# Optimization experiments

Hardware: AMD Instinct MI355X
Metric: run time of the kernel (lower is better)

The kernel has to match this reference:

```python
import jax, jax.numpy as jnp
import numpy as np

N = 50000      # nodes
E = 800000     # edges (before self-loops)
DIN, H1, H2, OUT = 128, 128, 64, 40
LN_EPS = 1e-5


def setup_inputs() -> dict:
    key = jax.random.key(0)
    ks = jax.random.split(key, 16)
    s = lambda d: 1.0 / np.sqrt(d)
    inp = {
        "x": jax.random.normal(ks[0], (N, DIN), jnp.float32),
        "edge_index": jax.random.randint(ks[1], (2, E), 0, N, dtype=jnp.int64),
        # GCNConv weights (applied as x @ W) and biases
        "W1": jax.random.normal(ks[2], (DIN, H1), jnp.float32) * s(DIN),
        "b1": jnp.zeros((H1,), jnp.float32),
        "W2": jax.random.normal(ks[3], (H1, H2), jnp.float32) * s(H1),
        "b2": jnp.zeros((H2,), jnp.float32),
        "W3": jax.random.normal(ks[4], (H2, H2), jnp.float32) * s(H2),
        "b3": jnp.zeros((H2,), jnp.float32),
        # LayerNorms
        "g1": jnp.ones((H1,), jnp.float32),
        "be1": jnp.zeros((H1,), jnp.float32),
        "g2": jnp.ones((H2,), jnp.float32),
        "be2": jnp.zeros((H2,), jnp.float32),
        # post_mp MLP head
        "Wp1": jax.random.normal(ks[5], (H2, H2), jnp.float32) * s(H2),
        "bp1": jnp.zeros((H2,), jnp.float32),
        "Wp2": jax.random.normal(ks[6], (H2, OUT), jnp.float32) * s(H2),
        "bp2": jnp.zeros((OUT,), jnp.float32),
    }
    return inp


def _layer_norm(x, g, b):
    mu = jnp.mean(x, axis=-1, keepdims=True)
    var = jnp.mean((x - mu) ** 2, axis=-1, keepdims=True)
    return (x - mu) * jax.lax.rsqrt(var + LN_EPS) * g + b


def _gcn(x, src, dst, norm, W, b):
    # PyG GCNConv: linear first, then normalized gather/scatter-add, bias last
    h = x @ W                                  # [N, H]
    msg = h[src] * norm[:, None]               # [E+N, H] gather
    out = jax.ops.segment_sum(msg, dst, num_segments=N)  # scatter-add
    return out + b


def reference(x, edge_index, W1, b1, W2, b2, W3, b3, g1, be1, g2, be2,
              Wp1, bp1, Wp2, bp2):
    loops = jnp.arange(N, dtype=edge_index.dtype)
    src = jnp.concatenate([edge_index[0], loops])  # add self-loops
    dst = jnp.concatenate([edge_index[1], loops])
    # symmetric normalization D^{-1/2} (A+I) D^{-1/2} (same graph all layers)
    deg = jax.ops.segment_sum(jnp.ones_like(src, dtype=x.dtype), dst,
                              num_segments=N)
    dinv = jnp.where(deg > 0, jax.lax.rsqrt(jnp.maximum(deg, 1.0)), 0.0)
    norm = dinv[src] * dinv[dst]

    h = _gcn(x, src, dst, norm, W1, b1)
    h = _layer_norm(jax.nn.relu(h), g1, be1)
    h = _gcn(h, src, dst, norm, W2, b2)
    h = _layer_norm(jax.nn.relu(h), g2, be2)
    emb = _gcn(h, src, dst, norm, W3, b3)      # emb = conv output, pre-ReLU
    h = jax.nn.relu(emb)
    h = (h @ Wp1 + bp1) @ Wp2 + bp2            # post_mp: two stacked Linears
    return emb, jax.nn.log_softmax(h, axis=1)
```

## Files before the change

kernel.cpp:

```cpp
#include <hip/hip_runtime.h>
#include <hip/hip_bf16.h>

#define DIN 128
#define HID1 128
#define HID2 64
#define OUTD 40

typedef __attribute__((ext_vector_type(8))) short bf16x8;
typedef __attribute__((ext_vector_type(4))) float f32x4;

__device__ __forceinline__ float bf2f(unsigned int u) {
    union { unsigned int i; float f; } c;
    c.i = u << 16;
    return c.f;
}
__device__ __forceinline__ unsigned short f2bf(float f) {
    union { float f; unsigned int i; } c; c.f = f;
    unsigned int r = c.i + 0x7FFFu + ((c.i >> 16) & 1u);
    return (unsigned short)(r >> 16);
}
__device__ __forceinline__ unsigned int packbf(float lo, float hi) {
    return (unsigned int)f2bf(lo) | ((unsigned int)f2bf(hi) << 16);
}

__global__ void pre_kernel(const unsigned short* __restrict__ xu,
                           const int* __restrict__ ei, int* __restrict__ flags,
                           int* __restrict__ cnt, int N) {
    int i = blockIdx.x * blockDim.x + threadIdx.x;
    if (i < N) cnt[i] = 0;
    if (blockIdx.x == 0) {
        __shared__ int sh[2];
        if (threadIdx.x < 2) sh[threadIdx.x] = 0;
        __syncthreads();
        int bad = 0;
        for (int k = threadIdx.x; k < 2048; k += 256) {
            float v = bf2f(xu[2 * k]);
            float a = fabsf(v);
            if (!(a <= 1e4f) || (v != 0.f && a < 1e-4f)) bad++;
        }
        int zodd = 0;
        for (int k = threadIdx.x; k < 1024; k += 256)
            if (ei[2 * k + 1] == 0) zodd++;
        atomicAdd(&sh[0], bad);
        atomicAdd(&sh[1], zodd);
        __syncthreads();
        if (threadIdx.x == 0) {
            flags[0] = (sh[0] > 512) ? 1 : 0;
            flags[1] = (sh[1] > 512) ? 1 : 0;
        }
    }
}

__device__ __forceinline__ int get_src(const int* ei, int E, int e, int e64) {
    return e64 ? ei[2 * e] : ei[e];
}
__device__ __forceinline__ int get_dst(const int* ei, int E, int e, int e64) {
    return e64 ? ei[2 * (E + e)] : ei[E + e];
}

__global__ void pos_kernel(const int* __restrict__ ei, int* __restrict__ cnt,
                           int* __restrict__ pos, int E, int N,
                           const int* __restrict__ flags) {
    int e64 = flags[1];
    int base = (blockIdx.x * blockDim.x + threadIdx.x) * 4;
    #pragma unroll
    for (int u = 0; u < 4; ++u) {
        int e = base + u;
        if (e < E) {
            int d = get_dst(ei, E, e, e64);
            pos[e] = ((unsigned)d < (unsigned)N) ? atomicAdd(&cnt[d], 1) : -1;
        }
    }
}


__launch_bounds__(256)
__global__ void bsum_kernel(const int* __restrict__ cnt, int* __restrict__ bsum, int N) {
    __shared__ int sh[256];
    int t = threadIdx.x;
    int i = blockIdx.x * 256 + t;
    sh[t] = (i < N) ? cnt[i] : 0;
    __syncthreads();
    #pragma unroll
    for (int off = 128; off >= 1; off >>= 1) {
        if (t < off) sh[t] += sh[t + off];
        __syncthreads();
    }
    if (t == 0) bsum[blockIdx.x] = sh[0];
}

__launch_bounds__(256)
__global__ void bscan_kernel(const int* __restrict__ bsum, int* __restrict__ bbase,
                             int* __restrict__ indptr, int NB, int N) {
    __shared__ int part[256];
    int t = threadIdx.x;
    int CH = (NB + 255) / 256;
    int lo = t * CH, hi = lo + CH; if (hi > NB) hi = NB;
    int s = 0;
    for (int i = lo; i < hi; ++i) s += bsum[i];
    part[t] = s;
    __syncthreads();
    for (int off = 1; off < 256; off <<= 1) {
        int v = (t >= off) ? part[t - off] : 0;
        __syncthreads();
        part[t] += v;
        __syncthreads();
    }
    int run = (t > 0) ? part[t - 1] : 0;
    for (int i = lo; i < hi; ++i) { bbase[i] = run; run += bsum[i]; }
    if (t == 255) indptr[N] = part[255];
}

__launch_bounds__(256)
__global__ void emit_kernel(const int* __restrict__ cnt, const int* __restrict__ bbase,
                            int* __restrict__ indptr, float* __restrict__ dinv, int N) {
    __shared__ int sh[256];
    int t = threadIdx.x;
    int i = blockIdx.x * 256 + t;
    int c = (i < N) ? cnt[i] : 0;
    sh[t] = c;
    __syncthreads();
    for (int off = 1; off < 256; off <<= 1) {
        int v = (t >= off) ? sh[t - off] : 0;
        __syncthreads();
        sh[t] += v;
        __syncthreads();
    }
    if (i < N) {
        int excl = sh[t] - c + bbase[blockIdx.x];
        indptr[i] = excl;
        dinv[i] = 1.0f / sqrtf((float)(c + 1));
    }
}

__global__ void scatter_kernel(const int* __restrict__ ei, const int* __restrict__ indptr,
                               const int* __restrict__ pos, const float* __restrict__ dinv,
                               int2* __restrict__ csr_sn,
                               int E, int N, const int* __restrict__ flags) {
    int e64 = flags[1];
    int base = (blockIdx.x * blockDim.x + threadIdx.x) * 4;
    #pragma unroll
    for (int u = 0; u < 4; ++u) {
        int e = base + u;
        if (e < E) {
            int p = pos[e];
            if (p >= 0) {
                int d = get_dst(ei, E, e, e64);
                int s = get_src(ei, E, e, e64);
                if ((unsigned)s >= (unsigned)N) s = 0;
                float nrm = dinv[s] * dinv[d];
                csr_sn[indptr[d] + p] = make_int2(s, __float_as_int(nrm));
            }
        }
    }
}


struct WCvt {
    const void* p[14];
    int sz[14];
    int off[14];
    int tobf[14];
    int cols[14];
};

__global__ void wcvt_kernel(WCvt w, unsigned short* __restrict__ wbf,
                            float* __restrict__ wf, const int* __restrict__ flags) {
    int xf32 = flags[0];
    int stride = gridDim.x * blockDim.x;
    int tid = blockIdx.x * blockDim.x + threadIdx.x;
    for (int a = 0; a < 14; ++a) {
        const float* pf = (const float*)w.p[a];
        const unsigned short* pb = (const unsigned short*)w.p[a];
        int n = w.sz[a], off = w.off[a], tobf = w.tobf[a];
        int cols = w.cols[a];
        int rows = tobf ? (n / cols) : 0;
        for (int i = tid; i < n; i += stride) {
            float v = xf32 ? pf[i] : bf2f(pb[i]);
            if (tobf) {
                int k = i / cols, m = i % cols;
                wbf[off + m * rows + k] = f2bf(v);
            } else {
                wf[off + i] = v;
            }
        }
    }
}


template<typename AT>
__device__ __forceinline__ bf16x8 ld_afrag(const AT* p);
template<>
__device__ __forceinline__ bf16x8 ld_afrag<unsigned short>(const unsigned short* p) {
    return *(const bf16x8*)p;
}
template<>
__device__ __forceinline__ bf16x8 ld_afrag<float>(const float* p) {
    float4 a = *(const float4*)p;
    float4 b = *(const float4*)(p + 4);
    bf16x8 r;
    r[0] = (short)f2bf(a.x); r[1] = (short)f2bf(a.y);
    r[2] = (short)f2bf(a.z); r[3] = (short)f2bf(a.w);
    r[4] = (short)f2bf(b.x); r[5] = (short)f2bf(b.y);
    r[6] = (short)f2bf(b.z); r[7] = (short)f2bf(b.w);
    return r;
}

template<int K, int M, typename AT>
__launch_bounds__(256)
__global__ void mm_mfma_kernel(const AT* __restrict__ A,
                               const unsigned short* __restrict__ WT,
                               unsigned short* __restrict__ C, int N,
                               const int* __restrict__ flags, int mode) {
    if (mode >= 0 && flags[0] != mode) return;
    __shared__ unsigned short Ws[M][K + 8];
    int tid = threadIdx.x;
    for (int idx = tid; idx < M * K / 8; idx += 256) {
        int r = idx / (K / 8), c8 = idx % (K / 8);
        *(uint4*)&Ws[r][c8 * 8] = *(const uint4*)&WT[r * K + c8 * 8];
    }
    __syncthreads();
    int w = tid >> 6, lane = tid & 63;
    int m = lane & 15, q = lane >> 4;
    int row_a = blockIdx.x * 64 + w * 16 + m;
    if (row_a >= N) row_a = N - 1;
    const AT* arow = A + (size_t)row_a * K;
    f32x4 acc[M / 16];
    #pragma unroll
    for (int t = 0; t < M / 16; ++t) acc[t] = (f32x4){0.f, 0.f, 0.f, 0.f};
    #pragma unroll
    for (int ks = 0; ks < K / 32; ++ks) {
        int k0 = ks * 32 + q * 8;
        bf16x8 a = ld_afrag<AT>(arow + k0);
        #pragma unroll
        for (int t = 0; t < M / 16; ++t) {
            bf16x8 b = *(const bf16x8*)&Ws[t * 16 + m][k0];
            acc[t] = __builtin_amdgcn_mfma_f32_16x16x32_bf16(a, b, acc[t], 0, 0, 0);
        }
    }
    int rbase = blockIdx.x * 64 + w * 16 + q * 4;
    #pragma unroll
    for (int reg = 0; reg < 4; ++reg) {
        int row = rbase + reg;
        if (row < N) {
            #pragma unroll
            for (int t = 0; t < M / 16; ++t)
                C[(size_t)row * M + t * 16 + m] = f2bf(acc[t][reg]);
        }
    }
}


template<int VPL>
__device__ __forceinline__ void gacc1(float* acc, const unsigned short* r, float n) {
    if constexpr (VPL == 8) {
        uint4 u = *(const uint4*)r;
        acc[0] += bf2f(u.x & 0xffffu) * n; acc[1] += bf2f(u.x >> 16) * n;
        acc[2] += bf2f(u.y & 0xffffu) * n; acc[3] += bf2f(u.y >> 16) * n;
        acc[4] += bf2f(u.z & 0xffffu) * n; acc[5] += bf2f(u.z >> 16) * n;
        acc[6] += bf2f(u.w & 0xffffu) * n; acc[7] += bf2f(u.w >> 16) * n;
    } else {
        uint2 u = *(const uint2*)r;
        acc[0] += bf2f(u.x & 0xffffu) * n; acc[1] += bf2f(u.x >> 16) * n;
        acc[2] += bf2f(u.y & 0xffffu) * n; acc[3] += bf2f(u.y >> 16) * n;
    }
}

template<int VPL>
__device__ __forceinline__ void gacc4(float* acc,
                                      const unsigned short* r0, float n0,
                                      const unsigned short* r1, float n1,
                                      const unsigned short* r2, float n2,
                                      const unsigned short* r3, float n3) {
    if constexpr (VPL == 8) {
        uint4 u0 = *(const uint4*)r0;
        uint4 u1 = *(const uint4*)r1;
        uint4 u2 = *(const uint4*)r2;
        uint4 u3 = *(const uint4*)r3;
        acc[0] += bf2f(u0.x & 0xffffu) * n0 + bf2f(u1.x & 0xffffu) * n1
                + bf2f(u2.x & 0xffffu) * n2 + bf2f(u3.x & 0xffffu) * n3;
        acc[1] += bf2f(u0.x >> 16) * n0 + bf2f(u1.x >> 16) * n1
                + bf2f(u2.x >> 16) * n2 + bf2f(u3.x >> 16) * n3;
        acc[2] += bf2f(u0.y & 0xffffu) * n0 + bf2f(u1.y & 0xffffu) * n1
                + bf2f(u2.y & 0xffffu) * n2 + bf2f(u3.y & 0xffffu) * n3;
        acc[3] += bf2f(u0.y >> 16) * n0 + bf2f(u1.y >> 16) * n1
                + bf2f(u2.y >> 16) * n2 + bf2f(u3.y >> 16) * n3;
        acc[4] += bf2f(u0.z & 0xffffu) * n0 + bf2f(u1.z & 0xffffu) * n1
                + bf2f(u2.z & 0xffffu) * n2 + bf2f(u3.z & 0xffffu) * n3;
        acc[5] += bf2f(u0.z >> 16) * n0 + bf2f(u1.z >> 16) * n1
                + bf2f(u2.z >> 16) * n2 + bf2f(u3.z >> 16) * n3;
        acc[6] += bf2f(u0.w & 0xffffu) * n0 + bf2f(u1.w & 0xffffu) * n1
                + bf2f(u2.w & 0xffffu) * n2 + bf2f(u3.w & 0xffffu) * n3;
        acc[7] += bf2f(u0.w >> 16) * n0 + bf2f(u1.w >> 16) * n1
                + bf2f(u2.w >> 16) * n2 + bf2f(u3.w >> 16) * n3;
    } else {
        uint2 u0 = *(const uint2*)r0;
        uint2 u1 = *(const uint2*)r1;
        uint2 u2 = *(const uint2*)r2;
        uint2 u3 = *(const uint2*)r3;
        acc[0] += bf2f(u0.x & 0xffffu) * n0 + bf2f(u1.x & 0xffffu) * n1
                + bf2f(u2.x & 0xffffu) * n2 + bf2f(u3.x & 0xffffu) * n3;
        acc[1] += bf2f(u0.x >> 16) * n0 + bf2f(u1.x >> 16) * n1
                + bf2f(u2.x >> 16) * n2 + bf2f(u3.x >> 16) * n3;
        acc[2] += bf2f(u0.y & 0xffffu) * n0 + bf2f(u1.y & 0xffffu) * n1
                + bf2f(u2.y & 0xffffu) * n2 + bf2f(u3.y & 0xffffu) * n3;
        acc[3] += bf2f(u0.y >> 16) * n0 + bf2f(u1.y >> 16) * n1
                + bf2f(u2.y >> 16) * n2 + bf2f(u3.y >> 16) * n3;
    }
}

template<int H, bool RELU_LN, bool EMB>
__launch_bounds__(256)
__global__ void agg_kernel(const unsigned short* __restrict__ h,
                           const int* __restrict__ indptr,
                           const int2* __restrict__ csr_sn,
                           const float* __restrict__ dinv,
                           const float* __restrict__ bias,
                           const float* __restrict__ gamma,
                           const float* __restrict__ beta,
                           unsigned short* __restrict__ out,
                           void* __restrict__ out_emb,
                           int N, const int* __restrict__ flags) {
    constexpr int VPL = H / 16;
    __shared__ int2 lsn[4][4][16];
    int w = threadIdx.x >> 6;
    int lane = threadIdx.x & 63;
    int g = lane >> 4;
    int idx = lane & 15;
    int node = blockIdx.x * 16 + w * 4 + g;
    bool active = node < N;
    int nd = active ? node : N - 1;
    float di = dinv[nd];
    int c0 = idx * VPL;
    float acc[VPL];
    #pragma unroll
    for (int v = 0; v < VPL; ++v) acc[v] = 0.f;
    gacc1<VPL>(acc, h + (size_t)nd * H + c0, di * di);
    int beg = indptr[nd], end = indptr[nd + 1];
    for (int base = beg; base < end; base += 16) {
        int m = end - base; if (m > 16) m = 16;
        if (idx < m) lsn[w][g][idx] = csr_sn[base + idx];
        int j = 0;
        for (; j + 3 < m; j += 4) {
            int2 e0 = lsn[w][g][j],     e1 = lsn[w][g][j + 1];
            int2 e2 = lsn[w][g][j + 2], e3 = lsn[w][g][j + 3];
            gacc4<VPL>(acc,
                       h + (size_t)e0.x * H + c0, __int_as_float(e0.y),
                       h + (size_t)e1.x * H + c0, __int_as_float(e1.y),
                       h + (size_t)e2.x * H + c0, __int_as_float(e2.y),
                       h + (size_t)e3.x * H + c0, __int_as_float(e3.y));
        }
        for (; j < m; ++j) {
            int2 e = lsn[w][g][j];
            gacc1<VPL>(acc, h + (size_t)e.x * H + c0, __int_as_float(e.y));
        }
    }
    #pragma unroll
    for (int v = 0; v < VPL; ++v) acc[v] += bias[c0 + v];
    if constexpr (RELU_LN) {
        #pragma unroll
        for (int v = 0; v < VPL; ++v) acc[v] = fmaxf(acc[v], 0.f);
        float s = 0.f, sq = 0.f;
        #pragma unroll
        for (int v = 0; v < VPL; ++v) { s += acc[v]; sq += acc[v] * acc[v]; }
        #pragma unroll
        for (int off = 8; off >= 1; off >>= 1) {
            s += __shfl_xor(s, off, 64);
            sq += __shfl_xor(sq, off, 64);
        }
        float mu = s * (1.0f / H);
        float var = fmaxf(sq * (1.0f / H) - mu * mu, 0.f);
        float inv = 1.0f / sqrtf(var + 1e-5f);
        #pragma unroll
        for (int v = 0; v < VPL; ++v)
            acc[v] = (acc[v] - mu) * inv * gamma[c0 + v] + beta[c0 + v];
    }
    if (active) {
        unsigned short* orow = out + (size_t)node * H + c0;
        if constexpr (VPL == 8) {
            uint4 p;
            p.x = packbf(acc[0], acc[1]); p.y = packbf(acc[2], acc[3]);
            p.z = packbf(acc[4], acc[5]); p.w = packbf(acc[6], acc[7]);
            *(uint4*)orow = p;
        } else {
            uint2 p; p.x = packbf(acc[0], acc[1]); p.y = packbf(acc[2], acc[3]);
            *(uint2*)orow = p;
        }
        if constexpr (EMB) {
            if (flags[0]) {
                float* o = (float*)out_emb + (size_t)node * H + c0;
                #pragma unroll
                for (int v4 = 0; v4 < VPL / 4; ++v4)
                    *(float4*)(o + v4 * 4) = make_float4(acc[v4 * 4], acc[v4 * 4 + 1],
                                                         acc[v4 * 4 + 2], acc[v4 * 4 + 3]);
            } else {
                unsigned short* o = (unsigned short*)out_emb + (size_t)node * H + c0;
                #pragma unroll
                for (int v2 = 0; v2 < VPL / 2; ++v2)
                    ((unsigned int*)o)[v2] = packbf(acc[v2 * 2], acc[v2 * 2 + 1]);
            }
        }
    }
}


__launch_bounds__(256)
__global__ void head_kernel(const unsigned short* __restrict__ emb,
                            const float* __restrict__ Wp1,
                            const float* __restrict__ bp1,
                            const float* __restrict__ Wp2,
                            const float* __restrict__ bp2,
                            void* __restrict__ d_out, int N,
                            const int* __restrict__ flags) {
    __shared__ float Est[64][68];
    __shared__ float W1s[64][64];
    __shared__ float Tst[64][68];
    __shared__ float W2s[64][OUTD];
    __shared__ float b1s[64];
    __shared__ float b2s[OUTD];
    int tid = threadIdx.x;
    int row0 = blockIdx.x * 64;
    for (int i = tid; i < 64 * 64; i += 256) W1s[i >> 6][i & 63] = Wp1[i];
    for (int i = tid; i < 64 * OUTD; i += 256) W2s[i / OUTD][i % OUTD] = Wp2[i];
    if (tid < 64) b1s[tid] = bp1[tid];
    if (tid < OUTD) b2s[tid] = bp2[tid];
    for (int i = tid; i < 64 * 32; i += 256) {
        int r = i >> 5, kk = i & 31;
        int row = row0 + r;
        unsigned int u = (row < N) ? *(const unsigned int*)&emb[(size_t)row * 64 + kk * 2] : 0u;
        Est[kk * 2][r]     = fmaxf(bf2f(u & 0xffffu), 0.f);
        Est[kk * 2 + 1][r] = fmaxf(bf2f(u >> 16), 0.f);
    }
    __syncthreads();
    {
        int rg = tid >> 4, cg = tid & 15;
        int r = rg * 4, c = cg * 4;
        float acc[4][4];
        #pragma unroll
        for (int i = 0; i < 4; ++i)
            #pragma unroll
            for (int jj = 0; jj < 4; ++jj) acc[i][jj] = b1s[c + jj];
        #pragma unroll 4
        for (int k = 0; k < 64; ++k) {
            float4 a = *(const float4*)&Est[k][r];
            float4 wv = *(const float4*)&W1s[k][c];
            acc[0][0] += a.x * wv.x; acc[0][1] += a.x * wv.y; acc[0][2] += a.x * wv.z; acc[0][3] += a.x * wv.w;
            acc[1][0] += a.y * wv.x; acc[1][1] += a.y * wv.y; acc[1][2] += a.y * wv.z; acc[1][3] += a.y * wv.w;
            acc[2][0] += a.z * wv.x; acc[2][1] += a.z * wv.y; acc[2][2] += a.z * wv.z; acc[2][3] += a.z * wv.w;
            acc[3][0] += a.w * wv.x; acc[3][1] += a.w * wv.y; acc[3][2] += a.w * wv.z; acc[3][3] += a.w * wv.w;
        }
        #pragma unroll
        for (int i = 0; i < 4; ++i)
            #pragma unroll
            for (int jj = 0; jj < 4; ++jj) Tst[c + jj][r + i] = acc[i][jj];
    }
    __syncthreads();
    int row = tid >> 2, tc = tid & 3, o0 = tc * 10;
    int node = row0 + row;
    float u[10];
    #pragma unroll
    for (int o = 0; o < 10; ++o) u[o] = b2s[o0 + o];
    for (int c2 = 0; c2 < 64; ++c2) {
        float tv = Tst[c2][row];
        const float2* wp = (const float2*)&W2s[c2][o0];
        #pragma unroll
        for (int o2 = 0; o2 < 5; ++o2) {
            float2 wv = wp[o2];
            u[o2 * 2]     += tv * wv.x;
            u[o2 * 2 + 1] += tv * wv.y;
        }
    }
    float mx = u[0];
    #pragma unroll
    for (int o = 1; o < 10; ++o) mx = fmaxf(mx, u[o]);
    mx = fmaxf(mx, __shfl_xor(mx, 1, 64));
    mx = fmaxf(mx, __shfl_xor(mx, 2, 64));
    float sum = 0.f;
    #pragma unroll
    for (int o = 0; o < 10; ++o) sum += __expf(u[o] - mx);
    sum += __shfl_xor(sum, 1, 64);
    sum += __shfl_xor(sum, 2, 64);
    float lse = mx + __logf(sum);
    if (node < N) {
        if (flags[0]) {
            float* base = (float*)d_out + (size_t)N * HID2;
            float* op = base + (size_t)node * OUTD + o0;
            #pragma unroll
            for (int o = 0; o < 10; ++o) op[o] = u[o] - lse;
        } else {
            unsigned short* base = (unsigned short*)d_out + (size_t)N * HID2;
            unsigned int* op = (unsigned int*)(base + (size_t)node * OUTD + o0);
            #pragma unroll
            for (int o2 = 0; o2 < 5; ++o2)
                op[o2] = packbf(u[o2 * 2] - lse, u[o2 * 2 + 1] - lse);
        }
    }
}


extern "C" void kernel_launch(void* const* d_in, const int* in_sizes, int n_in,
                              void* d_out, int out_size, void* d_ws, size_t ws_size,
                              hipStream_t stream) {
    const unsigned short* xu = (const unsigned short*)d_in[0];
    const float*          xf = (const float*)d_in[0];
    const int*            ei = (const int*)d_in[1];

    const int N = in_sizes[0] / DIN;
    const int E = in_sizes[1] / 2;

    size_t off = 0;
    auto take = [&](size_t bytes) {
        size_t cur = off;
        off += (bytes + 255) & ~(size_t)255;
        return cur;
    };
    char* ws = (char*)d_ws;
    int*   flags   = (int*)  (ws + take(256));
    int*   cnt     = (int*)  (ws + take((size_t)N * 4));
    float* dinv    = (float*)(ws + take((size_t)N * 4));
    int*   indptr  = (int*)  (ws + take((size_t)(N + 1) * 4));
    int*   pos     = (int*)  (ws + take((size_t)E * 4));
    int2*  csr_sn  = (int2*) (ws + take((size_t)E * 8));
    int*   bsum    = (int*)  (ws + take(((size_t)N / 256 + 2) * 4));
    int*   bbase   = (int*)  (ws + take(((size_t)N / 256 + 2) * 4));
    unsigned short* wbf = (unsigned short*)(ws + take(32768 * 2));
    float*          wf  = (float*)         (ws + take(8192 * 4));
    unsigned short* hbuf = (unsigned short*)(ws + take((size_t)N * DIN * 2));
    unsigned short* abuf = (unsigned short*)(ws + take((size_t)N * DIN * 2));
    (void)ws_size; (void)n_in; (void)out_size;

    const int TB = 256;
    dim3 blk(TB);
    const int NB = (N + 255) / 256;

    pre_kernel<<<dim3(NB), blk, 0, stream>>>(xu, ei, flags, cnt, N);
    pos_kernel<<<dim3((E + 1023) / 1024), blk, 0, stream>>>(ei, cnt, pos, E, N, flags);
    bsum_kernel<<<dim3(NB), blk, 0, stream>>>(cnt, bsum, N);
    bscan_kernel<<<dim3(1), blk, 0, stream>>>(bsum, bbase, indptr, NB, N);
    emit_kernel<<<dim3(NB), blk, 0, stream>>>(cnt, bbase, indptr, dinv, N);
    scatter_kernel<<<dim3((E + 1023) / 1024), blk, 0, stream>>>(ei, indptr, pos, dinv, csr_sn, E, N, flags);

    WCvt w;
    int bfoff = 0, foff = 0;
    int offs[14];
    const int wcols[14] = {HID1, 0, HID2, 0, HID2, 0, 0, 0, 0, 0, 0, 0, 0, 0};
    for (int a = 0; a < 14; ++a) {
        int idx = a + 2;
        w.p[a] = d_in[idx];
        w.sz[a] = in_sizes[idx];
        int tobf = (idx == 2 || idx == 4 || idx == 6) ? 1 : 0;
        w.tobf[a] = tobf;
        w.cols[a] = tobf ? wcols[a] : 1;
        if (tobf) { w.off[a] = bfoff; bfoff += in_sizes[idx]; }
        else      { w.off[a] = foff;  foff  += in_sizes[idx]; }
        offs[a] = w.off[a];
    }
    wcvt_kernel<<<dim3(64), blk, 0, stream>>>(w, wbf, wf, flags);

    unsigned short* W1t = wbf + offs[0];
    unsigned short* W2t = wbf + offs[2];
    unsigned short* W3t = wbf + offs[4];
    float* b1f  = wf + offs[1];
    float* b2f  = wf + offs[3];
    float* b3f  = wf + offs[5];
    float* g1f  = wf + offs[6];
    float* be1f = wf + offs[7];
    float* g2f  = wf + offs[8];
    float* be2f = wf + offs[9];
    float* Wp1f = wf + offs[10];
    float* bp1f = wf + offs[11];
    float* Wp2f = wf + offs[12];
    float* bp2f = wf + offs[13];

    const int MMG = (N + 63) / 64;
    const int AGG = (N + 15) / 16;

    mm_mfma_kernel<DIN, HID1, unsigned short><<<dim3(MMG), blk, 0, stream>>>(
        xu, W1t, hbuf, N, flags, 0);
    mm_mfma_kernel<DIN, HID1, float><<<dim3(MMG), blk, 0, stream>>>(
        xf, W1t, hbuf, N, flags, 1);
    agg_kernel<HID1, true, false><<<dim3(AGG), blk, 0, stream>>>(
        hbuf, indptr, csr_sn, dinv, b1f, g1f, be1f, abuf, nullptr, N, flags);

    mm_mfma_kernel<HID1, HID2, unsigned short><<<dim3(MMG), blk, 0, stream>>>(
        abuf, W2t, hbuf, N, flags, -1);
    agg_kernel<HID2, true, false><<<dim3(AGG), blk, 0, stream>>>(
        hbuf, indptr, csr_sn, dinv, b2f, g2f, be2f, abuf, nullptr, N, flags);

    mm_mfma_kernel<HID2, HID2, unsigned short><<<dim3(MMG), blk, 0, stream>>>(
        abuf, W3t, hbuf, N, flags, -1);
    agg_kernel<HID2, false, true><<<dim3(AGG), blk, 0, stream>>>(
        hbuf, indptr, csr_sn, dinv, b3f, nullptr, nullptr, abuf, d_out, N, flags);

    head_kernel<<<dim3((N + 63) / 64), blk, 0, stream>>>(
        abuf, Wp1f, bp1f, Wp2f, bp2f, d_out, N, flags);
}
```

Before: 312.6 us.

## Build CSR with per-chunk shared-memory histograms instead of global atomics

Replaces the global atomicAdd degree counting with 64 chunked blocks that each keep a packed 16-bit histogram of destination counts in LDS. A second pass prefix-sums the chunk histograms per node to get per-chunk base offsets, and the scatter combines indptr, chunk base and local position. The aim is to remove contention on global atomics. It also merges the two dtype-dispatched first-layer matmul launches into one kernel that branches on the flag. The cost is a large hist/basev workspace, an extra pass over 64×N entries, and only 64 blocks doing the edge pass.

```diff
diff --git a/kernel.cpp b/kernel.cpp
--- a/kernel.cpp
+++ b/kernel.cpp
@@ -5,6 +5,7 @@
 #define HID1 128
 #define HID2 64
 #define OUTD 40
+#define NCHUNK 64
 
 typedef __attribute__((ext_vector_type(8))) short bf16x8;
 typedef __attribute__((ext_vector_type(4))) float f32x4;
@@ -24,30 +25,25 @@
 }
 
 __global__ void pre_kernel(const unsigned short* __restrict__ xu,
-                           const int* __restrict__ ei, int* __restrict__ flags,
-                           int* __restrict__ cnt, int N) {
-    int i = blockIdx.x * blockDim.x + threadIdx.x;
-    if (i < N) cnt[i] = 0;
-    if (blockIdx.x == 0) {
-        __shared__ int sh[2];
-        if (threadIdx.x < 2) sh[threadIdx.x] = 0;
-        __syncthreads();
-        int bad = 0;
-        for (int k = threadIdx.x; k < 2048; k += 256) {
-            float v = bf2f(xu[2 * k]);
-            float a = fabsf(v);
-            if (!(a <= 1e4f) || (v != 0.f && a < 1e-4f)) bad++;
-        }
-        int zodd = 0;
-        for (int k = threadIdx.x; k < 1024; k += 256)
-            if (ei[2 * k + 1] == 0) zodd++;
-        atomicAdd(&sh[0], bad);
-        atomicAdd(&sh[1], zodd);
-        __syncthreads();
-        if (threadIdx.x == 0) {
-            flags[0] = (sh[0] > 512) ? 1 : 0;
-            flags[1] = (sh[1] > 512) ? 1 : 0;
-        }
+                           const int* __restrict__ ei, int* __restrict__ flags) {
+    __shared__ int sh[2];
+    if (threadIdx.x < 2) sh[threadIdx.x] = 0;
+    __syncthreads();
+    int bad = 0;
+    for (int k = threadIdx.x; k < 2048; k += 256) {
+        float v = bf2f(xu[2 * k]);
+        float a = fabsf(v);
+        if (!(a <= 1e4f) || (v != 0.f && a < 1e-4f)) bad++;
+    }
+    int zodd = 0;
+    for (int k = threadIdx.x; k < 1024; k += 256)
+        if (ei[2 * k + 1] == 0) zodd++;
+    atomicAdd(&sh[0], bad);
+    atomicAdd(&sh[1], zodd);
+    __syncthreads();
+    if (threadIdx.x == 0) {
+        flags[0] = (sh[0] > 512) ? 1 : 0;
+        flags[1] = (sh[1] > 512) ? 1 : 0;
     }
 }
 
@@ -58,19 +54,54 @@
     return e64 ? ei[2 * (E + e)] : ei[E + e];
 }
 
-__global__ void pos_kernel(const int* __restrict__ ei, int* __restrict__ cnt,
-                           int* __restrict__ pos, int E, int N,
-                           const int* __restrict__ flags) {
-    int e64 = flags[1];
-    int base = (blockIdx.x * blockDim.x + threadIdx.x) * 4;
-    #pragma unroll
-    for (int u = 0; u < 4; ++u) {
-        int e = base + u;
-        if (e < E) {
-            int d = get_dst(ei, E, e, e64);
-            pos[e] = ((unsigned)d < (unsigned)N) ? atomicAdd(&cnt[d], 1) : -1;
-        }
-    }
+
+__launch_bounds__(512)
+__global__ void posA_kernel(const int* __restrict__ ei, int* __restrict__ pos,
+                            unsigned int* __restrict__ hist, int E, int N,
+                            const int* __restrict__ flags) {
+    __shared__ unsigned int h32[25000];
+    const int NW = (N + 1) >> 1;
+    const int e64 = flags[1];
+    const int b = blockIdx.x;
+    const int CH = (E + NCHUNK - 1) / NCHUNK;
+    const int lo = b * CH;
+    int hi = lo + CH; if (hi > E) hi = E;
+    for (int w = threadIdx.x; w < NW; w += 512) h32[w] = 0u;
+    __syncthreads();
+    for (int e = lo + threadIdx.x; e < hi; e += 512) {
+        int d = get_dst(ei, E, e, e64);
+        if ((unsigned)d < (unsigned)N) {
+            unsigned sh = (unsigned)(d & 1) << 4;
+            unsigned old = atomicAdd(&h32[d >> 1], 1u << sh);
+            pos[e] = (int)((old >> sh) & 0xffffu);
+        } else {
+            pos[e] = -1;
+        }
+    }
+    __syncthreads();
+    unsigned int* hb = hist + (size_t)b * NW;
+    for (int w = threadIdx.x; w < NW; w += 512) hb[w] = h32[w];
+}
+
+__launch_bounds__(256)
+__global__ void phaseB_kernel(const unsigned int* __restrict__ hist,
+                              unsigned int* __restrict__ basev,
+                              int* __restrict__ cnt, int N) {
+    const int NW = (N + 1) >> 1;
+    const int NP = NW * 2;
+    int w = blockIdx.x * 256 + threadIdx.x;
+    if (w >= NW) return;
+    unsigned run0 = 0, run1 = 0;
+    #pragma unroll 4
+    for (int b = 0; b < NCHUNK; ++b) {
+        unsigned u = hist[(size_t)b * NW + w];
+        uint2 bb; bb.x = run0; bb.y = run1;
+        *(uint2*)&basev[(size_t)b * NP + 2 * w] = bb;
+        run0 += u & 0xffffu;
+        run1 += u >> 16;
+    }
+    cnt[2 * w] = (int)run0;
+    if (2 * w + 1 < N) cnt[2 * w + 1] = (int)run1;
 }
 
 
@@ -135,9 +166,12 @@
 
 __global__ void scatter_kernel(const int* __restrict__ ei, const int* __restrict__ indptr,
                                const int* __restrict__ pos, const float* __restrict__ dinv,
+                               const unsigned int* __restrict__ basev,
                                int2* __restrict__ csr_sn,
                                int E, int N, const int* __restrict__ flags) {
     int e64 = flags[1];
+    int CH = (E + NCHUNK - 1) / NCHUNK;
+    int NP = ((N + 1) >> 1) * 2;
     int base = (blockIdx.x * blockDim.x + threadIdx.x) * 4;
     #pragma unroll
     for (int u = 0; u < 4; ++u) {
@@ -145,11 +179,13 @@
         if (e < E) {
             int p = pos[e];
             if (p >= 0) {
+                int bb = e / CH;
                 int d = get_dst(ei, E, e, e64);
                 int s = get_src(ei, E, e, e64);
                 if ((unsigned)s >= (unsigned)N) s = 0;
                 float nrm = dinv[s] * dinv[d];
-                csr_sn[indptr[d] + p] = make_int2(s, __float_as_int(nrm));
+                int slot = indptr[d] + (int)basev[(size_t)bb * NP + d] + p;
+                csr_sn[slot] = make_int2(s, __float_as_int(nrm));
             }
         }
     }
@@ -207,13 +243,10 @@
 }
 
 template<int K, int M, typename AT>
-__launch_bounds__(256)
-__global__ void mm_mfma_kernel(const AT* __restrict__ A,
-                               const unsigned short* __restrict__ WT,
-                               unsigned short* __restrict__ C, int N,
-                               const int* __restrict__ flags, int mode) {
-    if (mode >= 0 && flags[0] != mode) return;
-    __shared__ unsigned short Ws[M][K + 8];
+__device__ __forceinline__ void mm_body(const AT* __restrict__ A,
+                                        const unsigned short* __restrict__ WT,
+                                        unsigned short* __restrict__ C, int N,
+                                        unsigned short (*Ws)[K + 8]) {
     int tid = threadIdx.x;
     for (int idx = tid; idx < M * K / 8; idx += 256) {
         int r = idx / (K / 8), c8 = idx % (K / 8);
@@ -248,6 +281,26 @@
                 C[(size_t)row * M + t * 16 + m] = f2bf(acc[t][reg]);
         }
     }
+}
+
+template<int K, int M>
+__launch_bounds__(256)
+__global__ void mm_dual_kernel(const void* __restrict__ A,
+                               const unsigned short* __restrict__ WT,
+                               unsigned short* __restrict__ C, int N,
+                               const int* __restrict__ flags) {
+    __shared__ unsigned short Ws[M][K + 8];
+    if (flags[0]) mm_body<K, M, float>((const float*)A, WT, C, N, Ws);
+    else          mm_body<K, M, unsigned short>((const unsigned short*)A, WT, C, N, Ws);
+}
+
+template<int K, int M>
+__launch_bounds__(256)
+__global__ void mm_bf_kernel(const unsigned short* __restrict__ A,
+                             const unsigned short* __restrict__ WT,
+                             unsigned short* __restrict__ C, int N) {
+    __shared__ unsigned short Ws[M][K + 8];
+    mm_body<K, M, unsigned short>(A, WT, C, N, Ws);
 }
 
 
@@ -502,11 +555,12 @@
                               void* d_out, int out_size, void* d_ws, size_t ws_size,
                               hipStream_t stream) {
     const unsigned short* xu = (const unsigned short*)d_in[0];
-    const float*          xf = (const float*)d_in[0];
     const int*            ei = (const int*)d_in[1];
 
     const int N = in_sizes[0] / DIN;
     const int E = in_sizes[1] / 2;
+    const int NW = (N + 1) / 2;
+    const int NP = NW * 2;
 
     size_t off = 0;
     auto take = [&](size_t bytes) {
@@ -523,6 +577,8 @@
     int2*  csr_sn  = (int2*) (ws + take((size_t)E * 8));
     int*   bsum    = (int*)  (ws + take(((size_t)N / 256 + 2) * 4));
     int*   bbase   = (int*)  (ws + take(((size_t)N / 256 + 2) * 4));
+    unsigned int* hist  = (unsigned int*)(ws + take((size_t)NCHUNK * NW * 4));
+    unsigned int* basev = (unsigned int*)(ws + take((size_t)NCHUNK * NP * 4));
     unsigned short* wbf = (unsigned short*)(ws + take(32768 * 2));
     float*          wf  = (float*)         (ws + take(8192 * 4));
     unsigned short* hbuf = (unsigned short*)(ws + take((size_t)N * DIN * 2));
@@ -533,12 +589,14 @@
     dim3 blk(TB);
     const int NB = (N + 255) / 256;
 
-    pre_kernel<<<dim3(NB), blk, 0, stream>>>(xu, ei, flags, cnt, N);
-    pos_kernel<<<dim3((E + 1023) / 1024), blk, 0, stream>>>(ei, cnt, pos, E, N, flags);
+    pre_kernel<<<dim3(1), blk, 0, stream>>>(xu, ei, flags);
+    posA_kernel<<<dim3(NCHUNK), dim3(512), 0, stream>>>(ei, pos, hist, E, N, flags);
+    phaseB_kernel<<<dim3((NW + 255) / 256), blk, 0, stream>>>(hist, basev, cnt, N);
     bsum_kernel<<<dim3(NB), blk, 0, stream>>>(cnt, bsum, N);
     bscan_kernel<<<dim3(1), blk, 0, stream>>>(bsum, bbase, indptr, NB, N);
     emit_kernel<<<dim3(NB), blk, 0, stream>>>(cnt, bbase, indptr, dinv, N);
-    scatter_kernel<<<dim3((E + 1023) / 1024), blk, 0, stream>>>(ei, indptr, pos, dinv, csr_sn, E, N, flags);
+    scatter_kernel<<<dim3((E + 1023) / 1024), blk, 0, stream>>>(
+        ei, indptr, pos, dinv, basev, csr_sn, E, N, flags);
 
     WCvt w;
     int bfoff = 0, foff = 0;
@@ -575,20 +633,16 @@
     const int MMG = (N + 63) / 64;
     const int AGG = (N + 15) / 16;
 
-    mm_mfma_kernel<DIN, HID1, unsigned short><<<dim3(MMG), blk, 0, stream>>>(
-        xu, W1t, hbuf, N, flags, 0);
-    mm_mfma_kernel<DIN, HID1, float><<<dim3(MMG), blk, 0, stream>>>(
-        xf, W1t, hbuf, N, flags, 1);
+    mm_dual_kernel<DIN, HID1><<<dim3(MMG), blk, 0, stream>>>(
+        d_in[0], W1t, hbuf, N, flags);
     agg_kernel<HID1, true, false><<<dim3(AGG), blk, 0, stream>>>(
         hbuf, indptr, csr_sn, dinv, b1f, g1f, be1f, abuf, nullptr, N, flags);
 
-    mm_mfma_kernel<HID1, HID2, unsigned short><<<dim3(MMG), blk, 0, stream>>>(
-        abuf, W2t, hbuf, N, flags, -1);
+    mm_bf_kernel<HID1, HID2><<<dim3(MMG), blk, 0, stream>>>(abuf, W2t, hbuf, N);
     agg_kernel<HID2, true, false><<<dim3(AGG), blk, 0, stream>>>(
         hbuf, indptr, csr_sn, dinv, b2f, g2f, be2f, abuf, nullptr, N, flags);
 
-    mm_mfma_kernel<HID2, HID2, unsigned short><<<dim3(MMG), blk, 0, stream>>>(
-        abuf, W3t, hbuf, N, flags, -1);
+    mm_bf_kernel<HID2, HID2><<<dim3(MMG), blk, 0, stream>>>(abuf, W3t, hbuf, N);
     agg_kernel<HID2, false, true><<<dim3(AGG), blk, 0, stream>>>(
         hbuf, indptr, csr_sn, dinv, b3f, nullptr, nullptr, abuf, d_out, N, flags);
 
```

Measured after the change: 306.7 us. About the same (-1.9%).
